# Kernel optimization log

Hardware: AMD Instinct MI355X
Metric: run time of the kernel (lower is better)

Reference implementation:

```python
import jax, jax.numpy as jnp
import numpy as np

B, N, T, H, KV = 8, 32, 1, 128, 4096
SCALE = H ** -0.5


def setup_inputs() -> dict:
    key = jax.random.key(0)
    kq, kk, kv_ = jax.random.split(key, 3)
    q = jax.random.normal(kq, (B, N, T, H), dtype=jnp.float32)
    k = jax.random.normal(kk, (B, N, KV, H), dtype=jnp.float32)
    v = jax.random.normal(kv_, (B, N, KV, H), dtype=jnp.float32)
    mask = jnp.zeros((B, 1, 1, KV), dtype=jnp.float32)
    return {"q": q, "k": k, "v": v, "mask": mask}


def reference(q, k, v, mask):
    # q: [B,N,T,H], k/v: [B,N,KV,H], mask: [B,1,1,KV]
    qs = q * jnp.asarray(SCALE, q.dtype)
    scores = jnp.einsum("bnth,bnkh->bntk", qs, k) + mask  # [B,N,T,KV]
    attn = jax.nn.softmax(scores, axis=-1)
    out = jnp.einsum("bntk,bnkh->bnth", attn, v)  # [B,N,T,H]
    return out
```

## Files before the change

### kernel.cpp

```cpp
#include <hip/hip_runtime.h>

#define BATCH 8
#define NHEADS 32
#define HDIM 128
#define KVLEN 4096
#define SCALE 0.08838834764831843f

constexpr int THREADS = 1024;
constexpr int GROUPS  = THREADS / 32;
constexpr int H4      = HDIM / 4;
constexpr int ITERS   = KVLEN / GROUPS;

__global__ __launch_bounds__(THREADS) void attn_decode_online(
    const float* __restrict__ q, const float* __restrict__ k,
    const float* __restrict__ v, const float* __restrict__ mask,
    float* __restrict__ out)
{
    __shared__ float s_m[GROUPS];
    __shared__ float s_l[GROUPS];
    __shared__ float s_acc[GROUPS * HDIM];

    const int bn  = blockIdx.x;
    const int b   = bn / NHEADS;
    const int tid = threadIdx.x;
    const int grp = tid >> 5;
    const int l32 = tid & 31;

    const float4* __restrict__ K4 = (const float4*)k;
    const float4* __restrict__ V4 = (const float4*)v;
    const float4* __restrict__ Q4 = (const float4*)q;

    const size_t base4 = (size_t)bn * KVLEN * H4;
    const float4 q4 = Q4[(size_t)bn * H4 + l32];
    const float* __restrict__ mrow = mask + (size_t)b * KVLEN;

    float m = -3.0e38f, l = 0.f;
    float a0 = 0.f, a1 = 0.f, a2 = 0.f, a3 = 0.f;

    #pragma unroll 2
    for (int i = 0; i < ITERS; ++i) {
        const int kk = grp + i * GROUPS;
        const size_t roff = base4 + (size_t)kk * H4 + l32;
        const float4 kv4 = K4[roff];
        const float4 vv4 = V4[roff];

        float p = q4.x * kv4.x + q4.y * kv4.y + q4.z * kv4.z + q4.w * kv4.w;
        p += __shfl_xor(p, 16);
        p += __shfl_xor(p, 8);
        p += __shfl_xor(p, 4);
        p += __shfl_xor(p, 2);
        p += __shfl_xor(p, 1);

        const float s    = p * SCALE + mrow[kk];
        const float mnew = fmaxf(m, s);
        const float c    = __expf(m - mnew);
        const float pe   = __expf(s - mnew);
        l  = l * c + pe;
        a0 = a0 * c + pe * vv4.x;
        a1 = a1 * c + pe * vv4.y;
        a2 = a2 * c + pe * vv4.z;
        a3 = a3 * c + pe * vv4.w;
        m  = mnew;
    }

    float* pp = s_acc + grp * HDIM + l32 * 4;
    pp[0] = a0; pp[1] = a1; pp[2] = a2; pp[3] = a3;
    if (l32 == 0) { s_m[grp] = m; s_l[grp] = l; }
    __syncthreads();

    if (tid < HDIM) {
        float M = -3.0e38f;
        #pragma unroll
        for (int g = 0; g < GROUPS; ++g) M = fmaxf(M, s_m[g]);
        float denom = 0.f, acc = 0.f;
        #pragma unroll
        for (int g = 0; g < GROUPS; ++g) {
            const float w = __expf(s_m[g] - M);
            denom += s_l[g] * w;
            acc   += s_acc[g * HDIM + tid] * w;
        }
        out[(size_t)bn * HDIM + tid] = acc / denom;
    }
}

extern "C" void kernel_launch(void* const* d_in, const int* in_sizes, int n_in,
                              void* d_out, int out_size, void* d_ws, size_t ws_size,
                              hipStream_t stream) {
    const float* q    = (const float*)d_in[0];
    const float* k    = (const float*)d_in[1];
    const float* v    = (const float*)d_in[2];
    const float* mask = (const float*)d_in[3];
    float* out = (float*)d_out;

    attn_decode_online<<<BATCH * NHEADS, THREADS, 0, stream>>>(q, k, v, mask, out);
}
```

Baseline: 185.5 us.

## Batch four KV rows per iteration with nontemporal loads and shared-memory mask

The online-softmax loop now processes four keys per group per iteration. All K/V loads for the batch are issued up front as nontemporal loads, and one max and rescale is done per batch instead of per key. The mask row is staged into shared memory once per block, so the loop no longer makes a scattered global read per key. This raises memory-level parallelism in a bandwidth-bound decode kernel, at the cost of more registers per thread at 1024 threads and an extra barrier.

```diff
diff --git a/kernel.cpp b/kernel.cpp
--- a/kernel.cpp
+++ b/kernel.cpp
@@ -6,16 +6,20 @@
 #define KVLEN 4096
 #define SCALE 0.08838834764831843f
 
+typedef float f32x4 __attribute__((ext_vector_type(4)));
+
 constexpr int THREADS = 1024;
 constexpr int GROUPS  = THREADS / 32;
 constexpr int H4      = HDIM / 4;
-constexpr int ITERS   = KVLEN / GROUPS;
+constexpr int KB      = 4;
+constexpr int MITERS  = KVLEN / (GROUPS * KB);
 
 __global__ __launch_bounds__(THREADS) void attn_decode_online(
     const float* __restrict__ q, const float* __restrict__ k,
     const float* __restrict__ v, const float* __restrict__ mask,
     float* __restrict__ out)
 {
+    __shared__ float s_mask[KVLEN];
     __shared__ float s_m[GROUPS];
     __shared__ float s_l[GROUPS];
     __shared__ float s_acc[GROUPS * HDIM];
@@ -26,40 +30,55 @@
     const int grp = tid >> 5;
     const int l32 = tid & 31;
 
-    const float4* __restrict__ K4 = (const float4*)k;
-    const float4* __restrict__ V4 = (const float4*)v;
-    const float4* __restrict__ Q4 = (const float4*)q;
+    const f32x4* __restrict__ K4 = (const f32x4*)k;
+    const f32x4* __restrict__ V4 = (const f32x4*)v;
+    const f32x4* __restrict__ Q4 = (const f32x4*)q;
+
+    ((f32x4*)s_mask)[tid] = ((const f32x4*)(mask + (size_t)b * KVLEN))[tid];
 
     const size_t base4 = (size_t)bn * KVLEN * H4;
-    const float4 q4 = Q4[(size_t)bn * H4 + l32];
-    const float* __restrict__ mrow = mask + (size_t)b * KVLEN;
+    const f32x4 q4 = Q4[(size_t)bn * H4 + l32];
+    __syncthreads();
 
     float m = -3.0e38f, l = 0.f;
     float a0 = 0.f, a1 = 0.f, a2 = 0.f, a3 = 0.f;
 
-    #pragma unroll 2
-    for (int i = 0; i < ITERS; ++i) {
-        const int kk = grp + i * GROUPS;
-        const size_t roff = base4 + (size_t)kk * H4 + l32;
-        const float4 kv4 = K4[roff];
-        const float4 vv4 = V4[roff];
+    for (int i = 0; i < MITERS; ++i) {
+        const int k0 = grp + i * (GROUPS * KB);
 
-        float p = q4.x * kv4.x + q4.y * kv4.y + q4.z * kv4.z + q4.w * kv4.w;
-        p += __shfl_xor(p, 16);
-        p += __shfl_xor(p, 8);
-        p += __shfl_xor(p, 4);
-        p += __shfl_xor(p, 2);
-        p += __shfl_xor(p, 1);
+        f32x4 kr[KB], vr[KB];
+        #pragma unroll
+        for (int j = 0; j < KB; ++j) {
+            const size_t roff = base4 + (size_t)(k0 + j * GROUPS) * H4 + l32;
+            kr[j] = __builtin_nontemporal_load(&K4[roff]);
+            vr[j] = __builtin_nontemporal_load(&V4[roff]);
+        }
 
-        const float s    = p * SCALE + mrow[kk];
-        const float mnew = fmaxf(m, s);
+        float s[KB];
+        #pragma unroll
+        for (int j = 0; j < KB; ++j) {
+            float p = kr[j].x * q4.x + kr[j].y * q4.y
+                    + kr[j].z * q4.z + kr[j].w * q4.w;
+            p += __shfl_xor(p, 16);
+            p += __shfl_xor(p, 8);
+            p += __shfl_xor(p, 4);
+            p += __shfl_xor(p, 2);
+            p += __shfl_xor(p, 1);
+            s[j] = p * SCALE + s_mask[k0 + j * GROUPS];
+        }
+
+        const float bmax = fmaxf(fmaxf(s[0], s[1]), fmaxf(s[2], s[3]));
+        const float mnew = fmaxf(m, bmax);
         const float c    = __expf(m - mnew);
-        const float pe   = __expf(s - mnew);
-        l  = l * c + pe;
-        a0 = a0 * c + pe * vv4.x;
-        a1 = a1 * c + pe * vv4.y;
-        a2 = a2 * c + pe * vv4.z;
-        a3 = a3 * c + pe * vv4.w;
+        float pe[KB];
+        #pragma unroll
+        for (int j = 0; j < KB; ++j) pe[j] = __expf(s[j] - mnew);
+
+        l  = l * c + (pe[0] + pe[1] + pe[2] + pe[3]);
+        a0 = a0 * c + pe[0]*vr[0].x + pe[1]*vr[1].x + pe[2]*vr[2].x + pe[3]*vr[3].x;
+        a1 = a1 * c + pe[0]*vr[0].y + pe[1]*vr[1].y + pe[2]*vr[2].y + pe[3]*vr[3].y;
+        a2 = a2 * c + pe[0]*vr[0].z + pe[1]*vr[1].z + pe[2]*vr[2].z + pe[3]*vr[3].z;
+        a3 = a3 * c + pe[0]*vr[0].w + pe[1]*vr[1].w + pe[2]*vr[2].w + pe[3]*vr[3].w;
         m  = mnew;
     }
 
```

Measured after the change: 163.8 us. 11.7% less time.
